# Kernel optimization log

Measured on AMD Instinct MI355X. Metric: run time of the kernel, lower is better.

The kernel has to match this reference:

```python
import jax, jax.numpy as jnp
import numpy as np
from jax import lax

HIDDEN = 16
DN = ('NCHW', 'OIHW', 'NCHW')

def setup_inputs() -> dict:
    key = jax.random.key(0)
    k1, k2, k3 = jax.random.split(key, 3)
    b, t, c, h, w = 8, 12, 5, 256, 256
    x = jax.random.normal(k1, (b, t, c, h, w), dtype=jnp.float32)
    # PyTorch-like init scale for conv weights
    W_cell = jax.random.normal(k2, (4 * HIDDEN, c + HIDDEN, 3, 3), dtype=jnp.float32) * 0.05
    b_cell = jnp.zeros((4 * HIDDEN,), dtype=jnp.float32)
    W_final = jax.random.normal(k3, (1, HIDDEN, 1, 1), dtype=jnp.float32) * 0.1
    b_final = jnp.zeros((1,), dtype=jnp.float32)
    return {"x": x, "W_cell": W_cell, "b_cell": b_cell,
            "W_final": W_final, "b_final": b_final}

def _cell_step(h_c, x_t, W_cell, b_cell):
    h_cur, c_cur = h_c
    combined = jnp.concatenate([x_t, h_cur], axis=1)          # [B, C+H, H, W]
    conv = lax.conv_general_dilated(combined, W_cell, (1, 1), 'SAME',
                                    dimension_numbers=DN)
    conv = conv + b_cell[None, :, None, None]                  # [B, 4H, H, W]
    cc_i, cc_f, cc_o, cc_g = jnp.split(conv, 4, axis=1)
    i = jax.nn.sigmoid(cc_i)
    f = jax.nn.sigmoid(cc_f)
    o = jax.nn.sigmoid(cc_o)
    g = jnp.tanh(cc_g)
    c_next = f * c_cur + i * g
    h_next = o * jnp.tanh(c_next)
    return h_next, c_next

def reference(x, W_cell, b_cell, W_final, b_final):
    b, t, c, hh, ww = x.shape
    h0 = jnp.zeros((b, HIDDEN, hh, ww), dtype=x.dtype)
    c0 = jnp.zeros((b, HIDDEN, hh, ww), dtype=x.dtype)
    xt = jnp.moveaxis(x, 1, 0)  # [T, B, C, H, W] for scan over time

    def step(carry, x_t):
        return _cell_step(carry, x_t, W_cell, b_cell), None

    (h_last, _), _ = lax.scan(step, (h0, c0), xt)
    out = lax.conv_general_dilated(h_last, W_final, (1, 1), 'SAME',
                                   dimension_numbers=DN)
    out = out + b_final[None, :, None, None]
    return out
```

## Files before the change

### kernel.cpp

```cpp
#include <hip/hip_runtime.h>
#include <math.h>

#define HIDDEN 16
#define CIN 5
#define BB 8
#define TT 12
#define HH 256
#define WW 256
#define TX 32
#define TY 8
#define HALO_X 34
#define HALO_Y 10
#define NPX (HALO_X * HALO_Y)
#define STRIDE 40
#define PTX 32
#define PTY 4
#define PHX 34
#define PHY 6
#define PNPX (PHX * PHY)
#define ROWSH 24
#define NTILES 4096
#define NBLK_PERSIST 1024
#define XSTEP (HH * WW * 8)
#define WSH (9 * 4 * 48 * 8)
#define WSH_PAD (WSH + 8)
#define TILE_SH (PNPX * ROWSH)
#define WOFF TILE_SH
#define ZOFF (TILE_SH + WSH)
#define SMSH (TILE_SH + WSH_PAD)

typedef __attribute__((ext_vector_type(8))) short bf16x8;
typedef __attribute__((ext_vector_type(4))) float floatx4;

__device__ __forceinline__ unsigned short f2bf(float f) {
    unsigned int u = __float_as_uint(f);
    u += 0x7fffu + ((u >> 16) & 1u);
    return (unsigned short)(u >> 16);
}
__device__ __forceinline__ float bf2f(unsigned short s) {
    return __uint_as_float(((unsigned int)s) << 16);
}
__device__ __forceinline__ float rcpf(float x) {
    float r;
    asm("v_rcp_f32 %0, %1" : "=v"(r) : "v"(x));
    return r;
}
__device__ __forceinline__ float fast_sigmoid(float x) {
    return rcpf(1.0f + __expf(-x));
}
__device__ __forceinline__ float fast_tanh(float x) {
    float e2 = __expf(-2.0f * fabsf(x));
    float t = (1.0f - e2) * rcpf(1.0f + e2);
    return copysignf(t, x);
}
__device__ __forceinline__ float leg_sigmoid(float x) { return 1.0f / (1.0f + __expf(-x)); }
__device__ __forceinline__ float leg_tanh(float x) {
    float e2 = __expf(-2.0f * fabsf(x));
    float t = (1.0f - e2) / (1.0f + e2);
    return copysignf(t, x);
}

__global__ void prep_w_kernel(const float* __restrict__ Wc,
                              unsigned short* __restrict__ Wfrag) {
    int i = blockIdx.x * 256 + threadIdx.x;
    if (i >= WSH_PAD) return;
    if (i >= WSH) { Wfrag[i] = 0; return; }
    int j    = i & 7;
    int t8   = i >> 3;
    int lane = t8 % 48;
    int t48  = t8 / 48;
    int g    = t48 & 3;
    int tap  = t48 >> 2;
    int k    = ((lane >> 4) << 3) + j;
    int col  = lane & 15;
    int o    = g * 16 + col;
    float w  = 0.0f;
    if (k < 21) {
        int ci_ref = (k < 16) ? (5 + k) : (k - 16);
        w = Wc[(o * 21 + ci_ref) * 9 + tap];
    }
    Wfrag[i] = f2bf(w);
}

__global__ void prep_x_kernel(const float* __restrict__ x,
                              unsigned short* __restrict__ xp) {
    size_t n = (size_t)blockIdx.x * 256 + threadIdx.x;
    const size_t TOTPX = (size_t)BB * TT * HH * WW;
    if (n >= TOTPX) return;
    size_t bt  = n / (size_t)(HH * WW);
    size_t pix = n - bt * (size_t)(HH * WW);
    const float* src = x + bt * (size_t)CIN * HH * WW + pix;
    unsigned short v[8];
    #pragma unroll
    for (int c = 0; c < CIN; ++c) v[c] = f2bf(src[(size_t)c * HH * WW]);
    v[5] = 0; v[6] = 0; v[7] = 0;
    *(uint4*)&xp[n * 8] = *(const uint4*)v;
}

__global__ void prep_flags_kernel(unsigned int* __restrict__ flags) {
    int i = blockIdx.x * 256 + threadIdx.x;
    if (i < NTILES) flags[i] = 0;
}

__global__ __launch_bounds__(256, 4)
void convlstm_persistent_kernel(const float* __restrict__ x,
                                const unsigned short* __restrict__ xp,
                                unsigned short* __restrict__ ha,
                                unsigned short* __restrict__ hbuf,
                                const unsigned short* __restrict__ Wfrag,
                                const float* __restrict__ bias,
                                const float* __restrict__ Wf,
                                const float* __restrict__ bfin,
                                float* __restrict__ out,
                                unsigned int* __restrict__ flags,
                                int use_xp) {
    __shared__ unsigned short sm[SMSH];

    const int tid  = threadIdx.x;
    const int lane = tid & 63;
    const int wave = tid >> 6;
    const int u    = lane & 15;
    const int quad = lane >> 4;
    const int bid  = (int)blockIdx.x;

    const int bb = bid >> 7;
    const int ty = (bid >> 1) & 63;
    const int y0 = ty * PTY;
    const int n0 = bid * 4;

    for (int i = tid; i < WSH_PAD / 8; i += 256)
        *(uint4*)&sm[WOFF + i * 8] = *(const uint4*)&Wfrag[i * 8];

    const int wbl   = (lane < 48) ? (WOFF + lane * 8) : ZOFF;
    const int wstep = (lane < 48) ? 384 : 0;

    int nb_dy = 0, nb_dx = 0;
    {
        int s  = lane + (lane >= 4 ? 1 : 0);
        nb_dy = s / 3 - 1;
        nb_dx = s - (s / 3) * 3 - 1;
    }

    const int sly = tid / PHX;
    const int slx = tid - sly * PHX;
    const int gy  = y0 + sly - 1;
    const bool yok = (gy >= 0) && (gy < HH);
    const int hbase_y = (bb * HH * WW + gy * WW) * HIDDEN;
    const int xbase_y = (bb * TT * HH * WW + gy * WW) * 8;

    float bg[4];
    #pragma unroll
    for (int g = 0; g < 4; ++g) bg[g] = bias[g * 16 + u];
    const float wfu = Wf[u];
    const float bf0 = bfin[0];

    int A[2];
    #pragma unroll
    for (int mh = 0; mh < 2; ++mh)
        A[mh] = (quad < 3) ? ((wave * PHX + mh * 16 + u) * ROWSH + quad * 8)
                           : ZOFF;
    const int msel = (quad < 3) ? ROWSH : 0;

    float cV0[2][4], cV1[2][4], cV2[2][4], cV3[2][4];
    #pragma unroll
    for (int m = 0; m < 2; ++m)
        #pragma unroll
        for (int r = 0; r < 4; ++r) {
            cV0[m][r] = 0.0f; cV1[m][r] = 0.0f;
            cV2[m][r] = 0.0f; cV3[m][r] = 0.0f;
        }

    #pragma unroll 1
    for (int t = 0; t < TT; ++t) {
        const unsigned short* h_in  = (t & 1) ? ha : hbuf;
        unsigned short*       h_out = (t & 1) ? hbuf : ha;
        const int first = (t == 0);
        const int last  = (t == TT - 1);

        #pragma unroll 1
        for (int v = 0; v < 4; ++v) {
            const int n  = n0 + v;
            const int tx = n & 7;
            const int x0 = tx * PTX;

            if (t > 0) {
                if (wave == 0) {
                    bool act = (lane < 8) && (tx + nb_dx >= 0) && (tx + nb_dx < 8)
                                          && (ty + nb_dy >= 0) && (ty + nb_dy < 64);
                    int nb = n + nb_dy * 8 + nb_dx;
                    const unsigned need = (unsigned)t;
                    for (;;) {
                        unsigned fv = act
                            ? __hip_atomic_load(&flags[nb], __ATOMIC_RELAXED,
                                                __HIP_MEMORY_SCOPE_AGENT)
                            : 0xFFFFFFFFu;
                        if (__all(fv >= need)) break;
                        __builtin_amdgcn_s_sleep(2);
                    }
                    if (tid == 0) __threadfence();
                }
                __syncthreads();
            }

            if (tid < PNPX) {
                unsigned short* row = &sm[tid * ROWSH];
                uint4 z = {0, 0, 0, 0};
                int gx = x0 + slx - 1;
                bool inb = yok && ((unsigned)gx < (unsigned)WW);
                if (inb && !first) {
                    const unsigned short* hp = h_in + hbase_y + gx * HIDDEN;
                    *(uint4*)&row[0] = *(const uint4*)&hp[0];
                    *(uint4*)&row[8] = *(const uint4*)&hp[8];
                } else {
                    *(uint4*)&row[0] = z;
                    *(uint4*)&row[8] = z;
                }
                if (use_xp) {
                    if (inb)
                        *(uint4*)&row[16] =
                            *(const uint4*)&xp[xbase_y + t * XSTEP + gx * 8];
                    else
                        *(uint4*)&row[16] = z;
                } else {
                    unsigned short vv[8];
                    #pragma unroll
                    for (int ci = 0; ci < CIN; ++ci) {
                        float f = 0.0f;
                        if (inb) f = x[(((size_t)bb * TT + t) * CIN + ci)
                                       * (size_t)(HH * WW) + gy * WW + gx];
                        vv[ci] = f2bf(f);
                    }
                    vv[5] = 0; vv[6] = 0; vv[7] = 0;
                    *(uint4*)&row[16] = *(const uint4*)vv;
                }
            }
            __syncthreads();

            floatx4 acc[2][4];
            #pragma unroll
            for (int mh = 0; mh < 2; ++mh)
                #pragma unroll
                for (int g = 0; g < 4; ++g)
                    acc[mh][g] = (floatx4){bg[g], bg[g], bg[g], bg[g]};

            #pragma unroll 3
            for (int tap = 0; tap < 9; ++tap) {
                int ky = tap / 3;
                int kx = tap - ky * 3;
                int ktap = ky * PHX + kx;
                bf16x8 bfr[4];
                #pragma unroll
                for (int g = 0; g < 4; ++g)
                    bfr[g] = *(const bf16x8*)&sm[wbl + (tap * 4 + g) * wstep];
                #pragma unroll
                for (int mh = 0; mh < 2; ++mh) {
                    bf16x8 af = *(const bf16x8*)&sm[A[mh] + ktap * msel];
                    #pragma unroll
                    for (int g = 0; g < 4; ++g)
                        acc[mh][g] = __builtin_amdgcn_mfma_f32_16x16x32_bf16(
                            af, bfr[g], acc[mh][g], 0, 0, 0);
                }
            }

            #pragma unroll
            for (int mh = 0; mh < 2; ++mh) {
                int py = y0 + wave;
                int col0 = mh * 16 + quad * 4;
                size_t gidx0 = ((size_t)bb * HH * WW + (size_t)py * WW + x0 + col0)
                               * HIDDEN + u;
                #pragma unroll
                for (int r = 0; r < 4; ++r) {
                    float ig = fast_sigmoid(acc[mh][0][r]);
                    float fg = fast_sigmoid(acc[mh][1][r]);
                    float og = fast_sigmoid(acc[mh][2][r]);
                    float gg = fast_tanh(acc[mh][3][r]);
                    float c_old = (v & 2) ? ((v & 1) ? cV3[mh][r] : cV2[mh][r])
                                          : ((v & 1) ? cV1[mh][r] : cV0[mh][r]);
                    float c_new = fg * c_old + ig * gg;
                    if (v & 2) { if (v & 1) cV3[mh][r] = c_new; else cV2[mh][r] = c_new; }
                    else       { if (v & 1) cV1[mh][r] = c_new; else cV0[mh][r] = c_new; }
                    float hval = og * fast_tanh(c_new);
                    if (last) {
                        float s = wfu * hval;
                        s += __shfl_xor(s, 1);
                        s += __shfl_xor(s, 2);
                        s += __shfl_xor(s, 4);
                        s += __shfl_xor(s, 8);
                        if (u == 0)
                            out[(size_t)bb * HH * WW + (size_t)py * WW + x0 + col0 + r]
                                = s + bf0;
                    } else {
                        h_out[gidx0 + (size_t)r * HIDDEN] = f2bf(hval);
                    }
                }
            }

            __syncthreads();
            if (!last && tid == 0) {
                __threadfence();
                __hip_atomic_store(&flags[n], (unsigned)(t + 1), __ATOMIC_RELAXED,
                                   __HIP_MEMORY_SCOPE_AGENT);
            }
        }
    }
}

__global__ __launch_bounds__(256, 5)
void convlstm_step_kernel(const float* __restrict__ x, int t,
                          const unsigned short* __restrict__ xp,
                          const unsigned short* __restrict__ h_in,
                          unsigned short* __restrict__ h_out,
                          float* __restrict__ c_state,
                          const unsigned short* __restrict__ Wfrag,
                          const float* __restrict__ bias,
                          int first, int use_xp) {
    __shared__ unsigned short tile[NPX * STRIDE];

    const int tid  = threadIdx.x;
    const int lane = tid & 63;
    const int wave = tid >> 6;
    const int x0 = blockIdx.x * TX;
    const int y0 = blockIdx.y * TY;
    const int bb = blockIdx.z;

    for (int i = tid; i < NPX; i += 256) {
        int ly = i / HALO_X;
        int lx = i - ly * HALO_X;
        int gy = y0 + ly - 1;
        int gx = x0 + lx - 1;
        bool inb = (gy >= 0 && gy < HH && gx >= 0 && gx < WW);
        unsigned short* row = &tile[i * STRIDE];
        uint4 z = {0, 0, 0, 0};
        if (inb && !first) {
            size_t hbase = ((size_t)bb * HH * WW + (size_t)gy * WW + gx) * HIDDEN;
            *(uint4*)&row[0] = *(const uint4*)&h_in[hbase];
            *(uint4*)&row[8] = *(const uint4*)&h_in[hbase + 8];
        } else {
            *(uint4*)&row[0] = z;
            *(uint4*)&row[8] = z;
        }
        if (use_xp) {
            if (inb) {
                size_t xb = (((size_t)bb * TT + t) * (size_t)(HH * WW)
                             + (size_t)gy * WW + gx) * 8;
                *(uint4*)&row[16] = *(const uint4*)&xp[xb];
            } else {
                *(uint4*)&row[16] = z;
            }
        } else {
            #pragma unroll
            for (int ci = 0; ci < CIN; ++ci) {
                float v = 0.0f;
                if (inb) v = x[(((size_t)bb * TT + t) * CIN + ci) * (size_t)(HH * WW)
                               + (size_t)gy * WW + gx];
                row[16 + ci] = f2bf(v);
            }
            row[21] = 0; row[22] = 0; row[23] = 0;
        }
        *(uint4*)&row[24] = z;
    }
    __syncthreads();

    const int u    = lane & 15;
    const int quad = lane >> 4;

    const unsigned short* wptr = (lane < 48) ? (Wfrag + lane * 8) : (Wfrag + WSH);
    const int wstep2 = (lane < 48) ? 384 : 0;

    float bg[4];
    #pragma unroll
    for (int g = 0; g < 4; ++g) bg[g] = bias[g * 16 + u];

    #pragma unroll 1
    for (int half = 0; half < 2; ++half) {
        floatx4 acc[2][4];
        int abase[2];
        #pragma unroll
        for (int mh = 0; mh < 2; ++mh) {
            int ml = half * 2 + mh;
            int m  = wave + ml * 4;
            int my = m >> 1;
            int mx = (m & 1) << 4;
            abase[mh] = (my * HALO_X + mx + u) * STRIDE + quad * 8;
            #pragma unroll
            for (int g = 0; g < 4; ++g)
                acc[mh][g] = (floatx4){bg[g], bg[g], bg[g], bg[g]};
        }

        #pragma unroll 3
        for (int tap = 0; tap < 9; ++tap) {
            int ky = tap / 3;
            int kx = tap - ky * 3;
            int toff = (ky * HALO_X + kx) * STRIDE;
            bf16x8 bfr[4];
            #pragma unroll
            for (int g = 0; g < 4; ++g)
                bfr[g] = *(const bf16x8*)&wptr[(tap * 4 + g) * wstep2];
            #pragma unroll
            for (int mh = 0; mh < 2; ++mh) {
                bf16x8 af = *(const bf16x8*)&tile[abase[mh] + toff];
                #pragma unroll
                for (int g = 0; g < 4; ++g)
                    acc[mh][g] = __builtin_amdgcn_mfma_f32_16x16x32_bf16(
                        af, bfr[g], acc[mh][g], 0, 0, 0);
            }
        }

        #pragma unroll
        for (int mh = 0; mh < 2; ++mh) {
            int ml = half * 2 + mh;
            int m  = wave + ml * 4;
            int my = m >> 1;
            int mx = (m & 1) << 4;
            int py = y0 + my;
            #pragma unroll
            for (int r = 0; r < 4; ++r) {
                int pxx = x0 + mx + quad * 4 + r;
                size_t idx = ((size_t)bb * HH * WW + (size_t)py * WW + pxx) * HIDDEN + u;
                float ig = leg_sigmoid(acc[mh][0][r]);
                float fg = leg_sigmoid(acc[mh][1][r]);
                float og = leg_sigmoid(acc[mh][2][r]);
                float gg = leg_tanh(acc[mh][3][r]);
                float c_old = first ? 0.0f : c_state[idx];
                float c_new = fg * c_old + ig * gg;
                c_state[idx] = c_new;
                h_out[idx] = f2bf(og * leg_tanh(c_new));
            }
        }
    }
}

__global__ void final_conv_kernel(const unsigned short* __restrict__ h,
                                  const float* __restrict__ Wf,
                                  const float* __restrict__ bf_,
                                  float* __restrict__ out) {
    int i = blockIdx.x * 256 + threadIdx.x;
    if (i >= BB * HH * WW) return;
    size_t base = (size_t)i * HIDDEN;
    uint4 v0 = *(const uint4*)&h[base];
    uint4 v1 = *(const uint4*)&h[base + 8];
    const unsigned short* p0 = (const unsigned short*)&v0;
    const unsigned short* p1 = (const unsigned short*)&v1;
    float s = bf_[0];
    #pragma unroll
    for (int k = 0; k < 8; ++k) s += Wf[k] * bf2f(p0[k]);
    #pragma unroll
    for (int k = 0; k < 8; ++k) s += Wf[8 + k] * bf2f(p1[k]);
    out[i] = s;
}

extern "C" void kernel_launch(void* const* d_in, const int* in_sizes, int n_in,
                              void* d_out, int out_size, void* d_ws, size_t ws_size,
                              hipStream_t stream) {
    const float* x  = (const float*)d_in[0];
    const float* Wc = (const float*)d_in[1];
    const float* bc = (const float*)d_in[2];
    const float* Wf = (const float*)d_in[3];
    const float* bf = (const float*)d_in[4];
    float* out = (float*)d_out;

    char* ws = (char*)d_ws;
    const size_t h_bytes = (size_t)BB * HH * WW * HIDDEN * 2;
    const size_t c_bytes = (size_t)BB * HH * WW * HIDDEN * 4;
    const size_t w_bytes = (size_t)WSH_PAD * 2;
    const size_t f_bytes = (size_t)NTILES * 4;
    const size_t x_bytes = (size_t)BB * TT * HH * WW * 8 * 2;

    unsigned short* h_a = (unsigned short*)(ws);
    unsigned short* h_b = (unsigned short*)(ws + h_bytes);
    float* c            = (float*)(ws + 2 * h_bytes);
    unsigned short* Wfr = (unsigned short*)(ws + 2 * h_bytes + c_bytes);
    unsigned int* flags = (unsigned int*)(ws + 2 * h_bytes + c_bytes + w_bytes);
    unsigned short* xp  = (unsigned short*)(ws + 2 * h_bytes + c_bytes + w_bytes + f_bytes);

    const int use_xp =
        (ws_size >= 2 * h_bytes + c_bytes + w_bytes + f_bytes + x_bytes) ? 1 : 0;

    prep_w_kernel<<<(WSH_PAD + 255) / 256, 256, 0, stream>>>(Wc, Wfr);
    prep_flags_kernel<<<(NTILES + 255) / 256, 256, 0, stream>>>(flags);
    if (use_xp) {
        size_t totpx = (size_t)BB * TT * HH * WW;
        prep_x_kernel<<<(int)((totpx + 255) / 256), 256, 0, stream>>>(x, xp);
    }

    int occ = 0;
    hipOccupancyMaxActiveBlocksPerMultiprocessor(&occ, convlstm_persistent_kernel,
                                                 256, 0);
    bool done = false;
    if (occ >= 4) {
        const unsigned short* xp_arg = use_xp ? xp : (const unsigned short*)0;
        int use_xp_arg = use_xp;
        void* kargs[] = {
            (void*)&x, (void*)&xp_arg, (void*)&h_a, (void*)&h_b,
            (void*)&Wfr, (void*)&bc, (void*)&Wf, (void*)&bf,
            (void*)&out, (void*)&flags, (void*)&use_xp_arg
        };
        if (hipLaunchCooperativeKernel((const void*)convlstm_persistent_kernel,
                                       dim3(NBLK_PERSIST, 1, 1), dim3(256, 1, 1),
                                       kargs, 0, stream) == hipSuccess)
            done = true;
    }

    if (!done) {
        dim3 grid(WW / TX, HH / TY, BB);
        dim3 block(256, 1, 1);
        const unsigned short* h_in = h_a;
        for (int t = 0; t < TT; ++t) {
            unsigned short* h_out = (t & 1) ? h_b : h_a;
            convlstm_step_kernel<<<grid, block, 0, stream>>>(
                x, t, use_xp ? xp : (const unsigned short*)0,
                h_in, h_out, c, Wfr, bc, (t == 0) ? 1 : 0, use_xp);
            h_in = h_out;
        }
        final_conv_kernel<<<(BB * HH * WW + 255) / 256, 256, 0, stream>>>(
            h_in, Wf, bf, out);
    }
}
```

Before: 715.5 us.

## Enlarge persistent ConvLSTM tiles to 64x8 with 512-thread blocks

Each persistent block now owns larger spatial tiles (64x8 instead of 32x4) and runs 512 threads, covering two tiles per time step instead of four. Each wave processes two row-pairs sequentially, keeping c-state in registers. The larger tiles shrink the halo overhead relative to useful pixels and cut the number of inter-tile flag handshakes per step. In exchange there are fewer, fatter blocks, more LDS per block, a serialized qq loop, and a row stride of 28 that may change LDS bank patterns.

```diff
diff --git a/kernel.cpp b/kernel.cpp
--- a/kernel.cpp
+++ b/kernel.cpp
@@ -13,14 +13,15 @@
 #define HALO_Y 10
 #define NPX (HALO_X * HALO_Y)
 #define STRIDE 40
-#define PTX 32
-#define PTY 4
-#define PHX 34
-#define PHY 6
+#define PTX 64
+#define PTY 8
+#define PHX 66
+#define PHY 10
 #define PNPX (PHX * PHY)
-#define ROWSH 24
-#define NTILES 4096
-#define NBLK_PERSIST 1024
+#define ROWSH 28
+#define NTILES 1024
+#define NBLK_PERSIST 512
+#define NTHR 512
 #define XSTEP (HH * WW * 8)
 #define WSH (9 * 4 * 48 * 8)
 #define WSH_PAD (WSH + 8)
@@ -102,7 +103,7 @@
     if (i < NTILES) flags[i] = 0;
 }
 
-__global__ __launch_bounds__(256, 4)
+__global__ __launch_bounds__(NTHR, 4)
 void convlstm_persistent_kernel(const float* __restrict__ x,
                                 const unsigned short* __restrict__ xp,
                                 unsigned short* __restrict__ ha,
@@ -123,12 +124,14 @@
     const int quad = lane >> 4;
     const int bid  = (int)blockIdx.x;
 
-    const int bb = bid >> 7;
-    const int ty = (bid >> 1) & 63;
-    const int y0 = ty * PTY;
-    const int n0 = bid * 4;
-
-    for (int i = tid; i < WSH_PAD / 8; i += 256)
+    const int n0  = bid * 2;
+    const int bb  = n0 >> 7;
+    const int q0  = n0 & 127;
+    const int ty  = q0 >> 2;
+    const int tx0 = q0 & 3;
+    const int y0  = ty * PTY;
+
+    for (int i = tid; i < WSH_PAD / 8; i += NTHR)
         *(uint4*)&sm[WOFF + i * 8] = *(const uint4*)&Wfrag[i * 8];
 
     const int wbl   = (lane < 48) ? (WOFF + lane * 8) : ZOFF;
@@ -141,33 +144,36 @@
         nb_dx = s - (s / 3) * 3 - 1;
     }
 
-    const int sly = tid / PHX;
-    const int slx = tid - sly * PHX;
-    const int gy  = y0 + sly - 1;
-    const bool yok = (gy >= 0) && (gy < HH);
-    const int hbase_y = (bb * HH * WW + gy * WW) * HIDDEN;
-    const int xbase_y = (bb * TT * HH * WW + gy * WW) * 8;
+    const int sly0 = tid / PHX;
+    const int slx0 = tid - sly0 * PHX;
+    const int i1   = tid + NTHR;
+    const int sly1 = i1 / PHX;
+    const int slx1 = i1 - sly1 * PHX;
+    const int gy0  = y0 + sly0 - 1;
+    const int gy1  = y0 + sly1 - 1;
+    const bool yok0 = (gy0 >= 0) && (gy0 < HH);
+    const bool yok1 = (gy1 >= 0) && (gy1 < HH);
+    const int hb0 = (bb * HH * WW + gy0 * WW) * HIDDEN;
+    const int hb1 = (bb * HH * WW + gy1 * WW) * HIDDEN;
+    const int xb0 = (bb * TT * HH * WW + gy0 * WW) * 8;
+    const int xb1 = (bb * TT * HH * WW + gy1 * WW) * 8;
 
     float bg[4];
     #pragma unroll
     for (int g = 0; g < 4; ++g) bg[g] = bias[g * 16 + u];
     const float wfu = Wf[u];
     const float bf0 = bfin[0];
-
-    int A[2];
-    #pragma unroll
-    for (int mh = 0; mh < 2; ++mh)
-        A[mh] = (quad < 3) ? ((wave * PHX + mh * 16 + u) * ROWSH + quad * 8)
-                           : ZOFF;
-    const int msel = (quad < 3) ? ROWSH : 0;
-
-    float cV0[2][4], cV1[2][4], cV2[2][4], cV3[2][4];
+    const int msel  = (quad < 3) ? ROWSH : 0;
+    const int mx    = (wave & 3) * 16;
+    const int rbase = (wave >> 2) * 4;
+
+    float cA0[2][4], cA1[2][4], cB0[2][4], cB1[2][4];
     #pragma unroll
     for (int m = 0; m < 2; ++m)
         #pragma unroll
         for (int r = 0; r < 4; ++r) {
-            cV0[m][r] = 0.0f; cV1[m][r] = 0.0f;
-            cV2[m][r] = 0.0f; cV3[m][r] = 0.0f;
+            cA0[m][r] = 0.0f; cA1[m][r] = 0.0f;
+            cB0[m][r] = 0.0f; cB1[m][r] = 0.0f;
         }
 
     #pragma unroll 1
@@ -178,16 +184,16 @@
         const int last  = (t == TT - 1);
 
         #pragma unroll 1
-        for (int v = 0; v < 4; ++v) {
+        for (int v = 0; v < 2; ++v) {
             const int n  = n0 + v;
-            const int tx = n & 7;
+            const int tx = tx0 + v;
             const int x0 = tx * PTX;
 
             if (t > 0) {
                 if (wave == 0) {
-                    bool act = (lane < 8) && (tx + nb_dx >= 0) && (tx + nb_dx < 8)
-                                          && (ty + nb_dy >= 0) && (ty + nb_dy < 64);
-                    int nb = n + nb_dy * 8 + nb_dx;
+                    bool act = (lane < 8) && (tx + nb_dx >= 0) && (tx + nb_dx < 4)
+                                          && (ty + nb_dy >= 0) && (ty + nb_dy < 32);
+                    int nb = n + nb_dy * 4 + nb_dx;
                     const unsigned need = (unsigned)t;
                     for (;;) {
                         unsigned fv = act
@@ -202,23 +208,21 @@
                 __syncthreads();
             }
 
-            if (tid < PNPX) {
+            {
                 unsigned short* row = &sm[tid * ROWSH];
                 uint4 z = {0, 0, 0, 0};
-                int gx = x0 + slx - 1;
-                bool inb = yok && ((unsigned)gx < (unsigned)WW);
+                int gx = x0 + slx0 - 1;
+                bool inb = yok0 && ((unsigned)gx < (unsigned)WW);
                 if (inb && !first) {
-                    const unsigned short* hp = h_in + hbase_y + gx * HIDDEN;
+                    const unsigned short* hp = h_in + hb0 + gx * HIDDEN;
                     *(uint4*)&row[0] = *(const uint4*)&hp[0];
                     *(uint4*)&row[8] = *(const uint4*)&hp[8];
                 } else {
-                    *(uint4*)&row[0] = z;
-                    *(uint4*)&row[8] = z;
+                    *(uint4*)&row[0] = z; *(uint4*)&row[8] = z;
                 }
                 if (use_xp) {
                     if (inb)
-                        *(uint4*)&row[16] =
-                            *(const uint4*)&xp[xbase_y + t * XSTEP + gx * 8];
+                        *(uint4*)&row[16] = *(const uint4*)&xp[xb0 + t * XSTEP + gx * 8];
                     else
                         *(uint4*)&row[16] = z;
                 } else {
@@ -227,70 +231,109 @@
                     for (int ci = 0; ci < CIN; ++ci) {
                         float f = 0.0f;
                         if (inb) f = x[(((size_t)bb * TT + t) * CIN + ci)
-                                       * (size_t)(HH * WW) + gy * WW + gx];
+                                       * (size_t)(HH * WW) + gy0 * WW + gx];
                         vv[ci] = f2bf(f);
                     }
                     vv[5] = 0; vv[6] = 0; vv[7] = 0;
                     *(uint4*)&row[16] = *(const uint4*)vv;
                 }
             }
+            if (tid < PNPX - NTHR) {
+                unsigned short* row = &sm[i1 * ROWSH];
+                uint4 z = {0, 0, 0, 0};
+                int gx = x0 + slx1 - 1;
+                bool inb = yok1 && ((unsigned)gx < (unsigned)WW);
+                if (inb && !first) {
+                    const unsigned short* hp = h_in + hb1 + gx * HIDDEN;
+                    *(uint4*)&row[0] = *(const uint4*)&hp[0];
+                    *(uint4*)&row[8] = *(const uint4*)&hp[8];
+                } else {
+                    *(uint4*)&row[0] = z; *(uint4*)&row[8] = z;
+                }
+                if (use_xp) {
+                    if (inb)
+                        *(uint4*)&row[16] = *(const uint4*)&xp[xb1 + t * XSTEP + gx * 8];
+                    else
+                        *(uint4*)&row[16] = z;
+                } else {
+                    unsigned short vv[8];
+                    #pragma unroll
+                    for (int ci = 0; ci < CIN; ++ci) {
+                        float f = 0.0f;
+                        if (inb) f = x[(((size_t)bb * TT + t) * CIN + ci)
+                                       * (size_t)(HH * WW) + gy1 * WW + gx];
+                        vv[ci] = f2bf(f);
+                    }
+                    vv[5] = 0; vv[6] = 0; vv[7] = 0;
+                    *(uint4*)&row[16] = *(const uint4*)vv;
+                }
+            }
             __syncthreads();
 
-            floatx4 acc[2][4];
-            #pragma unroll
-            for (int mh = 0; mh < 2; ++mh)
-                #pragma unroll
-                for (int g = 0; g < 4; ++g)
-                    acc[mh][g] = (floatx4){bg[g], bg[g], bg[g], bg[g]};
-
-            #pragma unroll 3
-            for (int tap = 0; tap < 9; ++tap) {
-                int ky = tap / 3;
-                int kx = tap - ky * 3;
-                int ktap = ky * PHX + kx;
-                bf16x8 bfr[4];
-                #pragma unroll
-                for (int g = 0; g < 4; ++g)
-                    bfr[g] = *(const bf16x8*)&sm[wbl + (tap * 4 + g) * wstep];
+            #pragma unroll 1
+            for (int qq = 0; qq < 2; ++qq) {
+                floatx4 acc[2][4];
+                int A[2];
                 #pragma unroll
                 for (int mh = 0; mh < 2; ++mh) {
-                    bf16x8 af = *(const bf16x8*)&sm[A[mh] + ktap * msel];
+                    int my = rbase + qq * 2 + mh;
+                    A[mh] = (quad < 3)
+                        ? ((my * PHX + mx + u) * ROWSH + quad * 8) : ZOFF;
                     #pragma unroll
                     for (int g = 0; g < 4; ++g)
-                        acc[mh][g] = __builtin_amdgcn_mfma_f32_16x16x32_bf16(
-                            af, bfr[g], acc[mh][g], 0, 0, 0);
-                }
-            }
-
-            #pragma unroll
-            for (int mh = 0; mh < 2; ++mh) {
-                int py = y0 + wave;
-                int col0 = mh * 16 + quad * 4;
-                size_t gidx0 = ((size_t)bb * HH * WW + (size_t)py * WW + x0 + col0)
-                               * HIDDEN + u;
+                        acc[mh][g] = (floatx4){bg[g], bg[g], bg[g], bg[g]};
+                }
+
+                #pragma unroll 3
+                for (int tap = 0; tap < 9; ++tap) {
+                    int ky = tap / 3;
+                    int kx = tap - ky * 3;
+                    int ktap = ky * PHX + kx;
+                    bf16x8 bfr[4];
+                    #pragma unroll
+                    for (int g = 0; g < 4; ++g)
+                        bfr[g] = *(const bf16x8*)&sm[wbl + (tap * 4 + g) * wstep];
+                    #pragma unroll
+                    for (int mh = 0; mh < 2; ++mh) {
+                        bf16x8 af = *(const bf16x8*)&sm[A[mh] + ktap * msel];
+                        #pragma unroll
+                        for (int g = 0; g < 4; ++g)
+                            acc[mh][g] = __builtin_amdgcn_mfma_f32_16x16x32_bf16(
+                                af, bfr[g], acc[mh][g], 0, 0, 0);
+                    }
+                }
+
                 #pragma unroll
-                for (int r = 0; r < 4; ++r) {
-                    float ig = fast_sigmoid(acc[mh][0][r]);
-                    float fg = fast_sigmoid(acc[mh][1][r]);
-                    float og = fast_sigmoid(acc[mh][2][r]);
-                    float gg = fast_tanh(acc[mh][3][r]);
-                    float c_old = (v & 2) ? ((v & 1) ? cV3[mh][r] : cV2[mh][r])
-                                          : ((v & 1) ? cV1[mh][r] : cV0[mh][r]);
-                    float c_new = fg * c_old + ig * gg;
-                    if (v & 2) { if (v & 1) cV3[mh][r] = c_new; else cV2[mh][r] = c_new; }
-                    else       { if (v & 1) cV1[mh][r] = c_new; else cV0[mh][r] = c_new; }
-                    float hval = og * fast_tanh(c_new);
-                    if (last) {
-                        float s = wfu * hval;
-                        s += __shfl_xor(s, 1);
-                        s += __shfl_xor(s, 2);
-                        s += __shfl_xor(s, 4);
-                        s += __shfl_xor(s, 8);
-                        if (u == 0)
-                            out[(size_t)bb * HH * WW + (size_t)py * WW + x0 + col0 + r]
-                                = s + bf0;
-                    } else {
-                        h_out[gidx0 + (size_t)r * HIDDEN] = f2bf(hval);
+                for (int mh = 0; mh < 2; ++mh) {
+                    int my = rbase + qq * 2 + mh;
+                    int py = y0 + my;
+                    int col0 = mx + quad * 4;
+                    size_t gidx0 = ((size_t)bb * HH * WW + (size_t)py * WW + x0 + col0)
+                                   * HIDDEN + u;
+                    #pragma unroll
+                    for (int r = 0; r < 4; ++r) {
+                        float ig = fast_sigmoid(acc[mh][0][r]);
+                        float fg = fast_sigmoid(acc[mh][1][r]);
+                        float og = fast_sigmoid(acc[mh][2][r]);
+                        float gg = fast_tanh(acc[mh][3][r]);
+                        float c_old = v ? (qq ? cB1[mh][r] : cB0[mh][r])
+                                        : (qq ? cA1[mh][r] : cA0[mh][r]);
+                        float c_new = fg * c_old + ig * gg;
+                        if (v) { if (qq) cB1[mh][r] = c_new; else cB0[mh][r] = c_new; }
+                        else   { if (qq) cA1[mh][r] = c_new; else cA0[mh][r] = c_new; }
+                        float hval = og * fast_tanh(c_new);
+                        if (last) {
+                            float s = wfu * hval;
+                            s += __shfl_xor(s, 1);
+                            s += __shfl_xor(s, 2);
+                            s += __shfl_xor(s, 4);
+                            s += __shfl_xor(s, 8);
+                            if (u == 0)
+                                out[(size_t)bb * HH * WW + (size_t)py * WW
+                                    + x0 + col0 + r] = s + bf0;
+                        } else {
+                            h_out[gidx0 + (size_t)r * HIDDEN] = f2bf(hval);
+                        }
                     }
                 }
             }
@@ -485,9 +528,9 @@
 
     int occ = 0;
     hipOccupancyMaxActiveBlocksPerMultiprocessor(&occ, convlstm_persistent_kernel,
-                                                 256, 0);
+                                                 NTHR, 0);
     bool done = false;
-    if (occ >= 4) {
+    if (occ >= 2) {
         const unsigned short* xp_arg = use_xp ? xp : (const unsigned short*)0;
         int use_xp_arg = use_xp;
         void* kargs[] = {
@@ -496,7 +539,7 @@
             (void*)&out, (void*)&flags, (void*)&use_xp_arg
         };
         if (hipLaunchCooperativeKernel((const void*)convlstm_persistent_kernel,
-                                       dim3(NBLK_PERSIST, 1, 1), dim3(256, 1, 1),
+                                       dim3(NBLK_PERSIST, 1, 1), dim3(NTHR, 1, 1),
                                        kargs, 0, stream) == hipSuccess)
             done = true;
     }
```

Result: no change. 713.5 us (-0.3%).

## Fuse two timesteps per sync using temporal tiling with halo recompute

Applied to the files above, without the earlier changes.

Restructures the persistent cooperative kernel so each block advances two LSTM timesteps per inter-block synchronization. It loads a 2-pixel halo and recomputes the intermediate h over a 34x10 region, then computes the second step from that tile. This halves the number of flag-based neighbor waits and the global h round trips. The costs are redundant halo compute, cell state stored in global memory (double-buffered c plus a per-block scratch) instead of registers, and weights now read from global/L1 rather than shared memory.

```diff
diff --git a/kernel.cpp b/kernel.cpp
--- a/kernel.cpp
+++ b/kernel.cpp
@@ -14,20 +14,24 @@
 #define NPX (HALO_X * HALO_Y)
 #define STRIDE 40
 #define PTX 32
-#define PTY 4
-#define PHX 34
-#define PHY 6
-#define PNPX (PHX * PHY)
-#define ROWSH 24
-#define NTILES 4096
-#define NBLK_PERSIST 1024
+#define PTY 8
+#define SHX 36
+#define SHY 12
+#define SNPX (SHX * SHY)
+#define THX 34
+#define THY 10
+#define TNPX (THX * THY)
+#define RS 24
+#define T_OFF (SNPX * RS)
+#define ZOFF (T_OFF + TNPX * RS)
+#define DOFF (ZOFF + 8)
+#define SMSH (DOFF + 24)
+#define NSS (TT / 2)
+#define NTILES 2048
+#define NBLK 1024
 #define XSTEP (HH * WW * 8)
 #define WSH (9 * 4 * 48 * 8)
 #define WSH_PAD (WSH + 8)
-#define TILE_SH (PNPX * ROWSH)
-#define WOFF TILE_SH
-#define ZOFF (TILE_SH + WSH)
-#define SMSH (TILE_SH + WSH_PAD)
 
 typedef __attribute__((ext_vector_type(8))) short bf16x8;
 typedef __attribute__((ext_vector_type(4))) float floatx4;
@@ -103,17 +107,18 @@
 }
 
 __global__ __launch_bounds__(256, 4)
-void convlstm_persistent_kernel(const float* __restrict__ x,
-                                const unsigned short* __restrict__ xp,
-                                unsigned short* __restrict__ ha,
-                                unsigned short* __restrict__ hbuf,
-                                const unsigned short* __restrict__ Wfrag,
-                                const float* __restrict__ bias,
-                                const float* __restrict__ Wf,
-                                const float* __restrict__ bfin,
-                                float* __restrict__ out,
-                                unsigned int* __restrict__ flags,
-                                int use_xp) {
+void convlstm_temporal_kernel(const unsigned short* __restrict__ xp,
+                              unsigned short* __restrict__ ha,
+                              unsigned short* __restrict__ hb,
+                              float* __restrict__ c0,
+                              float* __restrict__ c1,
+                              float* __restrict__ ctmp,
+                              const unsigned short* __restrict__ Wfrag,
+                              const float* __restrict__ bias,
+                              const float* __restrict__ Wf,
+                              const float* __restrict__ bfin,
+                              float* __restrict__ out,
+                              unsigned int* __restrict__ flags) {
     __shared__ unsigned short sm[SMSH];
 
     const int tid  = threadIdx.x;
@@ -123,30 +128,50 @@
     const int quad = lane >> 4;
     const int bid  = (int)blockIdx.x;
 
-    const int bb = bid >> 7;
-    const int ty = (bid >> 1) & 63;
-    const int y0 = ty * PTY;
-    const int n0 = bid * 4;
-
-    for (int i = tid; i < WSH_PAD / 8; i += 256)
-        *(uint4*)&sm[WOFF + i * 8] = *(const uint4*)&Wfrag[i * 8];
-
-    const int wbl   = (lane < 48) ? (WOFF + lane * 8) : ZOFF;
+    const int n0  = bid * 2;
+    const int bb  = n0 >> 8;
+    const int rem = n0 & 255;
+    const int ty  = rem >> 3;
+    const int tx0 = rem & 7;
+    const int y0  = ty * PTY;
+
+    if (tid == 0) { uint4 z = {0, 0, 0, 0}; *(uint4*)&sm[ZOFF] = z; }
+
+    const unsigned short* wptr = (lane < 48) ? (Wfrag + lane * 8) : (Wfrag + WSH);
     const int wstep = (lane < 48) ? 384 : 0;
 
     int nb_dy = 0, nb_dx = 0;
     {
-        int s  = lane + (lane >= 4 ? 1 : 0);
-        nb_dy = s / 3 - 1;
-        nb_dx = s - (s / 3) * 3 - 1;
-    }
-
-    const int sly = tid / PHX;
-    const int slx = tid - sly * PHX;
-    const int gy  = y0 + sly - 1;
-    const bool yok = (gy >= 0) && (gy < HH);
-    const int hbase_y = (bb * HH * WW + gy * WW) * HIDDEN;
-    const int xbase_y = (bb * TT * HH * WW + gy * WW) * 8;
+        int s8 = lane + (lane >= 4 ? 1 : 0);
+        nb_dy = s8 / 3 - 1;
+        nb_dx = s8 - (s8 / 3) * 3 - 1;
+    }
+
+    int scol_[2], hby_[2], xby_[2];
+    bool sv_[2], yos_[2];
+    #pragma unroll
+    for (int it = 0; it < 2; ++it) {
+        int i = tid + it * 256;
+        sv_[it] = (i < SNPX);
+        int rr = i / SHX;
+        scol_[it] = i - rr * SHX - 2;
+        int gy = y0 + rr - 2;
+        yos_[it] = ((unsigned)gy < (unsigned)HH);
+        hby_[it] = (bb * HH * WW + gy * WW) * HIDDEN;
+        xby_[it] = (bb * TT * HH * WW + gy * WW) * 8;
+    }
+    int tcolx_[2], xbyt_[2];
+    bool tv_[2], yot_[2];
+    #pragma unroll
+    for (int it = 0; it < 2; ++it) {
+        int j = tid + it * 256;
+        tv_[it] = (j < TNPX);
+        int rr = j / THX;
+        tcolx_[it] = j - rr * THX - 1;
+        int gy = y0 + rr - 1;
+        yot_[it] = ((unsigned)gy < (unsigned)HH);
+        xbyt_[it] = (bb * TT * HH * WW + gy * WW) * 8;
+    }
 
     float bg[4];
     #pragma unroll
@@ -154,47 +179,33 @@
     const float wfu = Wf[u];
     const float bf0 = bfin[0];
 
-    int A[2];
-    #pragma unroll
-    for (int mh = 0; mh < 2; ++mh)
-        A[mh] = (quad < 3) ? ((wave * PHX + mh * 16 + u) * ROWSH + quad * 8)
-                           : ZOFF;
-    const int msel = (quad < 3) ? ROWSH : 0;
-
-    float cV0[2][4], cV1[2][4], cV2[2][4], cV3[2][4];
-    #pragma unroll
-    for (int m = 0; m < 2; ++m)
-        #pragma unroll
-        for (int r = 0; r < 4; ++r) {
-            cV0[m][r] = 0.0f; cV1[m][r] = 0.0f;
-            cV2[m][r] = 0.0f; cV3[m][r] = 0.0f;
-        }
-
     #pragma unroll 1
-    for (int t = 0; t < TT; ++t) {
-        const unsigned short* h_in  = (t & 1) ? ha : hbuf;
-        unsigned short*       h_out = (t & 1) ? hbuf : ha;
-        const int first = (t == 0);
-        const int last  = (t == TT - 1);
+    for (int s = 0; s < NSS; ++s) {
+        const unsigned short* h_in = (s & 1) ? ha : hb;
+        unsigned short* h_out      = (s & 1) ? hb : ha;
+        const float* c_prev = (s & 1) ? c0 : c1;
+        float* c_cur        = (s & 1) ? c1 : c0;
+        const int first  = (s == 0);
+        const int lastss = (s == NSS - 1);
 
         #pragma unroll 1
-        for (int v = 0; v < 4; ++v) {
+        for (int v = 0; v < 2; ++v) {
             const int n  = n0 + v;
-            const int tx = n & 7;
+            const int tx = tx0 + v;
             const int x0 = tx * PTX;
 
-            if (t > 0) {
+            if (s > 0) {
                 if (wave == 0) {
-                    bool act = (lane < 8) && (tx + nb_dx >= 0) && (tx + nb_dx < 8)
-                                          && (ty + nb_dy >= 0) && (ty + nb_dy < 64);
+                    bool act = (lane < 8)
+                        && ((unsigned)(tx + nb_dx) < 8u)
+                        && ((unsigned)(ty + nb_dy) < 32u);
                     int nb = n + nb_dy * 8 + nb_dx;
-                    const unsigned need = (unsigned)t;
                     for (;;) {
                         unsigned fv = act
                             ? __hip_atomic_load(&flags[nb], __ATOMIC_RELAXED,
                                                 __HIP_MEMORY_SCOPE_AGENT)
                             : 0xFFFFFFFFu;
-                        if (__all(fv >= need)) break;
+                        if (__all(fv >= (unsigned)s)) break;
                         __builtin_amdgcn_s_sleep(2);
                     }
                     if (tid == 0) __threadfence();
@@ -202,103 +213,184 @@
                 __syncthreads();
             }
 
-            if (tid < PNPX) {
-                unsigned short* row = &sm[tid * ROWSH];
-                uint4 z = {0, 0, 0, 0};
-                int gx = x0 + slx - 1;
-                bool inb = yok && ((unsigned)gx < (unsigned)WW);
-                if (inb && !first) {
-                    const unsigned short* hp = h_in + hbase_y + gx * HIDDEN;
-                    *(uint4*)&row[0] = *(const uint4*)&hp[0];
-                    *(uint4*)&row[8] = *(const uint4*)&hp[8];
-                } else {
-                    *(uint4*)&row[0] = z;
-                    *(uint4*)&row[8] = z;
-                }
-                if (use_xp) {
+            #pragma unroll
+            for (int it = 0; it < 2; ++it) {
+                if (sv_[it]) {
+                    unsigned short* rp = &sm[(tid + it * 256) * RS];
+                    uint4 z = {0, 0, 0, 0};
+                    int gx = x0 + scol_[it];
+                    bool inb = yos_[it] && ((unsigned)gx < (unsigned)WW);
+                    if (inb && !first) {
+                        const unsigned short* hp = h_in + hby_[it] + gx * HIDDEN;
+                        *(uint4*)&rp[0] = *(const uint4*)&hp[0];
+                        *(uint4*)&rp[8] = *(const uint4*)&hp[8];
+                    } else {
+                        *(uint4*)&rp[0] = z; *(uint4*)&rp[8] = z;
+                    }
                     if (inb)
-                        *(uint4*)&row[16] =
-                            *(const uint4*)&xp[xbase_y + t * XSTEP + gx * 8];
+                        *(uint4*)&rp[16] =
+                            *(const uint4*)&xp[xby_[it] + (2 * s) * XSTEP + gx * 8];
                     else
-                        *(uint4*)&row[16] = z;
-                } else {
-                    unsigned short vv[8];
-                    #pragma unroll
-                    for (int ci = 0; ci < CIN; ++ci) {
-                        float f = 0.0f;
-                        if (inb) f = x[(((size_t)bb * TT + t) * CIN + ci)
-                                       * (size_t)(HH * WW) + gy * WW + gx];
-                        vv[ci] = f2bf(f);
-                    }
-                    vv[5] = 0; vv[6] = 0; vv[7] = 0;
-                    *(uint4*)&row[16] = *(const uint4*)vv;
+                        *(uint4*)&rp[16] = z;
+                }
+            }
+            #pragma unroll
+            for (int it = 0; it < 2; ++it) {
+                if (tv_[it]) {
+                    unsigned short* rp = &sm[T_OFF + (tid + it * 256) * RS];
+                    uint4 z = {0, 0, 0, 0};
+                    int gx = x0 + tcolx_[it];
+                    bool inb = yot_[it] && ((unsigned)gx < (unsigned)WW);
+                    if (inb)
+                        *(uint4*)&rp[16] =
+                            *(const uint4*)&xp[xbyt_[it] + (2 * s + 1) * XSTEP + gx * 8];
+                    else
+                        *(uint4*)&rp[16] = z;
                 }
             }
             __syncthreads();
 
-            floatx4 acc[2][4];
-            #pragma unroll
-            for (int mh = 0; mh < 2; ++mh)
+            #pragma unroll 1
+            for (int k = 0; k < 8; ++k) {
+                int idx = wave + (k << 2);
+                if (idx >= 30) break;
+                int rq   = idx / 3;
+                int band = idx - rq * 3;
+                int row  = rq - 1;
+                int col0 = band * 16 - 1;
+                int acol = col0 + u;
+                bool aval = (acol <= 32);
+                int A0, tmul;
+                if (quad < 3 && aval) {
+                    A0 = ((row + 1) * SHX + (acol + 1)) * RS + quad * 8;
+                    tmul = RS;
+                } else { A0 = ZOFF; tmul = 0; }
+
+                floatx4 acc[4];
                 #pragma unroll
                 for (int g = 0; g < 4; ++g)
-                    acc[mh][g] = (floatx4){bg[g], bg[g], bg[g], bg[g]};
-
-            #pragma unroll 3
-            for (int tap = 0; tap < 9; ++tap) {
-                int ky = tap / 3;
-                int kx = tap - ky * 3;
-                int ktap = ky * PHX + kx;
-                bf16x8 bfr[4];
+                    acc[g] = (floatx4){bg[g], bg[g], bg[g], bg[g]};
+
+                #pragma unroll 3
+                for (int tap = 0; tap < 9; ++tap) {
+                    int ky = tap / 3;
+                    int kx = tap - ky * 3;
+                    bf16x8 bfr[4];
+                    #pragma unroll
+                    for (int g = 0; g < 4; ++g)
+                        bfr[g] = *(const bf16x8*)&wptr[(tap * 4 + g) * wstep];
+                    bf16x8 af = *(const bf16x8*)&sm[A0 + (ky * SHX + kx) * tmul];
+                    #pragma unroll
+                    for (int g = 0; g < 4; ++g)
+                        acc[g] = __builtin_amdgcn_mfma_f32_16x16x32_bf16(
+                            af, bfr[g], acc[g], 0, 0, 0);
+                }
+
+                int gy = y0 + row;
+                bool yin = ((unsigned)gy < (unsigned)HH);
                 #pragma unroll
-                for (int g = 0; g < 4; ++g)
-                    bfr[g] = *(const bf16x8*)&sm[wbl + (tap * 4 + g) * wstep];
+                for (int r = 0; r < 4; ++r) {
+                    int tcol = col0 + quad * 4 + r;
+                    bool cval = (tcol <= 32);
+                    int gx = x0 + tcol;
+                    bool inb = yin && ((unsigned)gx < (unsigned)WW);
+                    float ig = fast_sigmoid(acc[0][r]);
+                    float fg = fast_sigmoid(acc[1][r]);
+                    float og = fast_sigmoid(acc[2][r]);
+                    float gg = fast_tanh(acc[3][r]);
+                    float c_old = 0.0f;
+                    if (!first && inb && cval)
+                        c_old = c_prev[(bb * HH * WW + gy * WW + gx) * HIDDEN + u];
+                    float c_new = fg * c_old + ig * gg;
+                    if (cval)
+                        ctmp[bid * (TNPX * HIDDEN)
+                             + ((row + 1) * THX + tcol + 1) * HIDDEN + u] = c_new;
+                    unsigned short hs = inb ? f2bf(og * fast_tanh(c_new))
+                                            : (unsigned short)0;
+                    int tw = cval ? (T_OFF + ((row + 1) * THX + tcol + 1) * RS + u)
+                                  : (DOFF + u);
+                    sm[tw] = hs;
+                }
+            }
+            __syncthreads();
+
+            #pragma unroll 1
+            for (int half = 0; half < 2; ++half) {
+                floatx4 acc[2][4];
+                int A[2];
                 #pragma unroll
                 for (int mh = 0; mh < 2; ++mh) {
-                    bf16x8 af = *(const bf16x8*)&sm[A[mh] + ktap * msel];
+                    int m   = wave + (half * 2 + mh) * 4;
+                    int my  = m >> 1;
+                    int mxx = (m & 1) << 4;
+                    A[mh] = (quad < 3)
+                        ? (T_OFF + (my * THX + mxx + u) * RS + quad * 8) : ZOFF;
                     #pragma unroll
                     for (int g = 0; g < 4; ++g)
-                        acc[mh][g] = __builtin_amdgcn_mfma_f32_16x16x32_bf16(
-                            af, bfr[g], acc[mh][g], 0, 0, 0);
-                }
-            }
-
-            #pragma unroll
-            for (int mh = 0; mh < 2; ++mh) {
-                int py = y0 + wave;
-                int col0 = mh * 16 + quad * 4;
-                size_t gidx0 = ((size_t)bb * HH * WW + (size_t)py * WW + x0 + col0)
-                               * HIDDEN + u;
+                        acc[mh][g] = (floatx4){bg[g], bg[g], bg[g], bg[g]};
+                }
+                const int msel = (quad < 3) ? RS : 0;
+
+                #pragma unroll 3
+                for (int tap = 0; tap < 9; ++tap) {
+                    int ky = tap / 3;
+                    int kx = tap - ky * 3;
+                    int toff = (ky * THX + kx) * msel;
+                    bf16x8 bfr[4];
+                    #pragma unroll
+                    for (int g = 0; g < 4; ++g)
+                        bfr[g] = *(const bf16x8*)&wptr[(tap * 4 + g) * wstep];
+                    #pragma unroll
+                    for (int mh = 0; mh < 2; ++mh) {
+                        bf16x8 af = *(const bf16x8*)&sm[A[mh] + toff];
+                        #pragma unroll
+                        for (int g = 0; g < 4; ++g)
+                            acc[mh][g] = __builtin_amdgcn_mfma_f32_16x16x32_bf16(
+                                af, bfr[g], acc[mh][g], 0, 0, 0);
+                    }
+                }
+
                 #pragma unroll
-                for (int r = 0; r < 4; ++r) {
-                    float ig = fast_sigmoid(acc[mh][0][r]);
-                    float fg = fast_sigmoid(acc[mh][1][r]);
-                    float og = fast_sigmoid(acc[mh][2][r]);
-                    float gg = fast_tanh(acc[mh][3][r]);
-                    float c_old = (v & 2) ? ((v & 1) ? cV3[mh][r] : cV2[mh][r])
-                                          : ((v & 1) ? cV1[mh][r] : cV0[mh][r]);
-                    float c_new = fg * c_old + ig * gg;
-                    if (v & 2) { if (v & 1) cV3[mh][r] = c_new; else cV2[mh][r] = c_new; }
-                    else       { if (v & 1) cV1[mh][r] = c_new; else cV0[mh][r] = c_new; }
-                    float hval = og * fast_tanh(c_new);
-                    if (last) {
-                        float s = wfu * hval;
-                        s += __shfl_xor(s, 1);
-                        s += __shfl_xor(s, 2);
-                        s += __shfl_xor(s, 4);
-                        s += __shfl_xor(s, 8);
-                        if (u == 0)
-                            out[(size_t)bb * HH * WW + (size_t)py * WW + x0 + col0 + r]
-                                = s + bf0;
-                    } else {
-                        h_out[gidx0 + (size_t)r * HIDDEN] = f2bf(hval);
+                for (int mh = 0; mh < 2; ++mh) {
+                    int m   = wave + (half * 2 + mh) * 4;
+                    int my  = m >> 1;
+                    int mxx = (m & 1) << 4;
+                    int py  = y0 + my;
+                    #pragma unroll
+                    for (int r = 0; r < 4; ++r) {
+                        int cl  = mxx + quad * 4 + r;
+                        int pxx = x0 + cl;
+                        float ig = fast_sigmoid(acc[mh][0][r]);
+                        float fg = fast_sigmoid(acc[mh][1][r]);
+                        float og = fast_sigmoid(acc[mh][2][r]);
+                        float gg = fast_tanh(acc[mh][3][r]);
+                        float c_old = ctmp[bid * (TNPX * HIDDEN)
+                                           + ((my + 1) * THX + cl + 1) * HIDDEN + u];
+                        float c_new = fg * c_old + ig * gg;
+                        size_t gidx = ((size_t)bb * HH * WW + (size_t)py * WW + pxx)
+                                      * HIDDEN + u;
+                        float hval = og * fast_tanh(c_new);
+                        if (lastss) {
+                            float sred = wfu * hval;
+                            sred += __shfl_xor(sred, 1);
+                            sred += __shfl_xor(sred, 2);
+                            sred += __shfl_xor(sred, 4);
+                            sred += __shfl_xor(sred, 8);
+                            if (u == 0)
+                                out[(size_t)bb * HH * WW + (size_t)py * WW + pxx]
+                                    = sred + bf0;
+                        } else {
+                            c_cur[gidx] = c_new;
+                            h_out[gidx] = f2bf(hval);
+                        }
                     }
                 }
             }
 
             __syncthreads();
-            if (!last && tid == 0) {
+            if (!lastss && tid == 0) {
                 __threadfence();
-                __hip_atomic_store(&flags[n], (unsigned)(t + 1), __ATOMIC_RELAXED,
+                __hip_atomic_store(&flags[n], (unsigned)(s + 1), __ATOMIC_RELAXED,
                                    __HIP_MEMORY_SCOPE_AGENT);
             }
         }
@@ -460,56 +552,71 @@
     float* out = (float*)d_out;
 
     char* ws = (char*)d_ws;
-    const size_t h_bytes = (size_t)BB * HH * WW * HIDDEN * 2;
-    const size_t c_bytes = (size_t)BB * HH * WW * HIDDEN * 4;
-    const size_t w_bytes = (size_t)WSH_PAD * 2;
-    const size_t f_bytes = (size_t)NTILES * 4;
-    const size_t x_bytes = (size_t)BB * TT * HH * WW * 8 * 2;
-
-    unsigned short* h_a = (unsigned short*)(ws);
-    unsigned short* h_b = (unsigned short*)(ws + h_bytes);
-    float* c            = (float*)(ws + 2 * h_bytes);
-    unsigned short* Wfr = (unsigned short*)(ws + 2 * h_bytes + c_bytes);
-    unsigned int* flags = (unsigned int*)(ws + 2 * h_bytes + c_bytes + w_bytes);
-    unsigned short* xp  = (unsigned short*)(ws + 2 * h_bytes + c_bytes + w_bytes + f_bytes);
-
-    const int use_xp =
-        (ws_size >= 2 * h_bytes + c_bytes + w_bytes + f_bytes + x_bytes) ? 1 : 0;
-
-    prep_w_kernel<<<(WSH_PAD + 255) / 256, 256, 0, stream>>>(Wc, Wfr);
-    prep_flags_kernel<<<(NTILES + 255) / 256, 256, 0, stream>>>(flags);
-    if (use_xp) {
+    const size_t h_bytes  = (size_t)BB * HH * WW * HIDDEN * 2;
+    const size_t c_bytes  = (size_t)BB * HH * WW * HIDDEN * 4;
+    const size_t ct_bytes = (size_t)NBLK * TNPX * HIDDEN * 4;
+    const size_t w_bytes  = (size_t)WSH_PAD * 2;
+    const size_t f_bytes  = (size_t)NTILES * 4;
+    const size_t x_bytes  = (size_t)BB * TT * HH * WW * 8 * 2;
+
+    unsigned short* h_a  = (unsigned short*)(ws);
+    unsigned short* h_b  = (unsigned short*)(ws + h_bytes);
+    float* c0p           = (float*)(ws + 2 * h_bytes);
+    float* c1p           = (float*)(ws + 2 * h_bytes + c_bytes);
+    float* ctmp          = (float*)(ws + 2 * h_bytes + 2 * c_bytes);
+    unsigned short* Wfr  = (unsigned short*)(ws + 2 * h_bytes + 2 * c_bytes + ct_bytes);
+    unsigned int* flags  = (unsigned int*)(ws + 2 * h_bytes + 2 * c_bytes + ct_bytes + w_bytes);
+    unsigned short* xp   = (unsigned short*)(ws + 2 * h_bytes + 2 * c_bytes + ct_bytes
+                                             + w_bytes + f_bytes);
+    const size_t need_temporal =
+        2 * h_bytes + 2 * c_bytes + ct_bytes + w_bytes + f_bytes + x_bytes;
+
+    bool done = false;
+    if (ws_size >= need_temporal) {
+        prep_w_kernel<<<(WSH_PAD + 255) / 256, 256, 0, stream>>>(Wc, Wfr);
+        prep_flags_kernel<<<(NTILES + 255) / 256, 256, 0, stream>>>(flags);
         size_t totpx = (size_t)BB * TT * HH * WW;
         prep_x_kernel<<<(int)((totpx + 255) / 256), 256, 0, stream>>>(x, xp);
-    }
-
-    int occ = 0;
-    hipOccupancyMaxActiveBlocksPerMultiprocessor(&occ, convlstm_persistent_kernel,
-                                                 256, 0);
-    bool done = false;
-    if (occ >= 4) {
-        const unsigned short* xp_arg = use_xp ? xp : (const unsigned short*)0;
-        int use_xp_arg = use_xp;
-        void* kargs[] = {
-            (void*)&x, (void*)&xp_arg, (void*)&h_a, (void*)&h_b,
-            (void*)&Wfr, (void*)&bc, (void*)&Wf, (void*)&bf,
-            (void*)&out, (void*)&flags, (void*)&use_xp_arg
-        };
-        if (hipLaunchCooperativeKernel((const void*)convlstm_persistent_kernel,
-                                       dim3(NBLK_PERSIST, 1, 1), dim3(256, 1, 1),
-                                       kargs, 0, stream) == hipSuccess)
-            done = true;
+
+        int occ = 0;
+        hipOccupancyMaxActiveBlocksPerMultiprocessor(&occ, convlstm_temporal_kernel,
+                                                     256, 0);
+        if (occ >= 4) {
+            void* kargs[] = {
+                (void*)&xp, (void*)&h_a, (void*)&h_b, (void*)&c0p, (void*)&c1p,
+                (void*)&ctmp, (void*)&Wfr, (void*)&bc, (void*)&Wf, (void*)&bf,
+                (void*)&out, (void*)&flags
+            };
+            if (hipLaunchCooperativeKernel((const void*)convlstm_temporal_kernel,
+                                           dim3(NBLK, 1, 1), dim3(256, 1, 1),
+                                           kargs, 0, stream) == hipSuccess)
+                done = true;
+        }
     }
 
     if (!done) {
+        unsigned short* lh_a = (unsigned short*)(ws);
+        unsigned short* lh_b = (unsigned short*)(ws + h_bytes);
+        float* lc            = (float*)(ws + 2 * h_bytes);
+        unsigned short* lWfr = (unsigned short*)(ws + 2 * h_bytes + c_bytes);
+        unsigned short* lxp  = (unsigned short*)(ws + 2 * h_bytes + c_bytes + w_bytes);
+        const int use_xp =
+            (ws_size >= 2 * h_bytes + c_bytes + w_bytes + x_bytes) ? 1 : 0;
+
+        prep_w_kernel<<<(WSH_PAD + 255) / 256, 256, 0, stream>>>(Wc, lWfr);
+        if (use_xp) {
+            size_t totpx = (size_t)BB * TT * HH * WW;
+            prep_x_kernel<<<(int)((totpx + 255) / 256), 256, 0, stream>>>(x, lxp);
+        }
+
         dim3 grid(WW / TX, HH / TY, BB);
         dim3 block(256, 1, 1);
-        const unsigned short* h_in = h_a;
+        const unsigned short* h_in = lh_a;
         for (int t = 0; t < TT; ++t) {
-            unsigned short* h_out = (t & 1) ? h_b : h_a;
+            unsigned short* h_out = (t & 1) ? lh_b : lh_a;
             convlstm_step_kernel<<<grid, block, 0, stream>>>(
-                x, t, use_xp ? xp : (const unsigned short*)0,
-                h_in, h_out, c, Wfr, bc, (t == 0) ? 1 : 0, use_xp);
+                x, t, use_xp ? lxp : (const unsigned short*)0,
+                h_in, h_out, lc, lWfr, bc, (t == 0) ? 1 : 0, use_xp);
             h_in = h_out;
         }
         final_conv_kernel<<<(BB * HH * WW + 255) / 256, 256, 0, stream>>>(
```

New measurement: 759.8 us. +6.2%, slower.
